# Kernel tuning notes

Measured on AMD Instinct MI355X. Metric: run time of the kernel, lower is better.

The kernel has to match this reference:

```python
import jax, jax.numpy as jnp
import numpy as np
import itertools

NBX = NBY = 6
NUM_BLOCKS = NBX * NBY

def _build_adj():
    adj = []
    for i, j in itertools.product(range(NBX), range(NBY)):
        for dx, dy in [(-1, 0), (0, -1), (0, 1), (1, 0)]:
            x, y = i + dx, j + dy
            if 0 <= x < NBX and 0 <= y < NBY:
                adj.append((j * NBX + i, y * NBX + x))
    return np.array(adj, dtype=np.int32)

ADJ = _build_adj()                                   # [E=120, 2] (src, dst)
NUM_EDGES = ADJ.shape[0]
# composition structure: edge e' can be extended by edge e iff dst(e') == src(e)
COMP = (ADJ[:, 1][:, None] == ADJ[:, 0][None, :]).astype(np.float32)  # [E, E]
MAX_PATH_LEN = NUM_BLOCKS                            # 36 fixed-point iterations


def setup_inputs() -> dict:
    key = jax.random.key(0)
    ks = jax.random.split(key, 10)
    w = lambda k, shape: jax.random.normal(k, shape, jnp.float32) * 0.05
    d = {}
    d["image"] = jax.random.normal(ks[0], (1024, 1, 32, 32), jnp.float32)
    d["conv1_w"] = w(ks[1], (32, 1, 5, 5));   d["conv1_b"] = jnp.zeros((32,), jnp.float32)
    d["conv2_w"] = w(ks[2], (32, 32, 5, 5));  d["conv2_b"] = jnp.zeros((32,), jnp.float32)
    d["conv3_w"] = w(ks[3], (64, 32, 5, 5));  d["conv3_b"] = jnp.zeros((64,), jnp.float32)
    d["conv4_w"] = w(ks[4], (64, 64, 5, 5));  d["conv4_b"] = jnp.zeros((64,), jnp.float32)
    d["ep_w1"] = w(ks[5], (256, 256));        d["ep_b1"] = jnp.zeros((256,), jnp.float32)
    d["ep_w2"] = w(ks[6], (NUM_BLOCKS, 256)); d["ep_b2"] = jnp.zeros((NUM_BLOCKS,), jnp.float32)
    d["conn_w1"] = w(ks[7], (256, 256));      d["conn_b1"] = jnp.zeros((256,), jnp.float32)
    d["conn_w2"] = w(ks[8], (NUM_EDGES, 256)); d["conn_b2"] = jnp.zeros((NUM_EDGES,), jnp.float32)
    return d


def _conv(x, w, b):
    y = jax.lax.conv_general_dilated(x, w, (1, 1), 'VALID',
                                     dimension_numbers=('NCHW', 'OIHW', 'NCHW'))
    return y + b[None, :, None, None]


def _pool2(x):
    return jax.lax.reduce_window(x, -jnp.inf, jax.lax.max,
                                 (1, 1, 2, 2), (1, 1, 2, 2), 'VALID')


def reference(image, conv1_w, conv1_b, conv2_w, conv2_b, conv3_w, conv3_b,
              conv4_w, conv4_b, ep_w1, ep_b1, ep_w2, ep_b2,
              conn_w1, conn_b1, conn_w2, conn_b2):
    # --- CNN feature extractor (NCHW, torch-flatten order) ---
    x = _conv(image, conv1_w, conv1_b)      # [B,32,28,28]
    x = _conv(x, conv2_w, conv2_b)          # [B,32,24,24]
    x = _pool2(x)                           # [B,32,12,12]
    x = _conv(x, conv3_w, conv3_b)          # [B,64,8,8]
    x = _conv(x, conv4_w, conv4_b)          # [B,64,4,4]
    x = _pool2(x)                           # [B,64,2,2]
    emb = x.reshape(x.shape[0], -1)         # [B,256]

    # --- heads ---
    conn = jax.nn.sigmoid(jax.nn.relu(emb @ conn_w1.T + conn_b1) @ conn_w2.T + conn_b2)  # [B,E]
    ep = jax.nn.sigmoid(jax.nn.relu(emb @ ep_w1.T + ep_b1) @ ep_w2.T + ep_b2)            # [B,36]

    # --- recursive path building under DAMP semiring (add=clipped sum, mult=product) ---
    comp = jnp.asarray(COMP)                # [E,E]: dst(e')==src(e)
    def step(carry, _):
        old, recent = carry
        # extend_path/extend_path_cond: new symbol is the edge itself, prob = (sum_paths_ending_at_src) * p_edge
        new = jnp.clip(recent @ comp, 0.0, 1.0) * conn   # [B,E]
        merged = jnp.clip(old + new, 0.0, 1.0)           # merge (|) with DAMP add
        return (merged, new), None
    (merged, _), _ = jax.lax.scan(step, (conn, conn), None, length=MAX_PATH_LEN)

    # is_endpoint: apply_if with first_index_check / last_index_check (semiring mult)
    src = jnp.asarray(ADJ[:, 0])
    dst = jnp.asarray(ADJ[:, 1])
    paths = merged * ep[:, src] * ep[:, dst]             # [B,E]
    return paths[:, 0]
```

## Files before the change

### kernel.cpp

```cpp
#include <hip/hip_runtime.h>
#include <math.h>

typedef __attribute__((ext_vector_type(8))) short short8;
typedef __attribute__((ext_vector_type(4))) float float4v;
typedef __attribute__((ext_vector_type(4))) unsigned short ushort4v;

static __device__ __forceinline__ unsigned short f2bf(float f) {
    union { float f; unsigned u; } v; v.f = f;
    unsigned u = v.u;
    return (unsigned short)((u + 0x7fffu + ((u >> 16) & 1u)) >> 16);
}
static __device__ __forceinline__ float bf2f(unsigned short h) {
    union { unsigned u; float f; } v; v.u = ((unsigned)h) << 16;
    return v.f;
}
static __device__ __forceinline__ unsigned pk2(float a, float b) {
    return (unsigned)f2bf(a) | ((unsigned)f2bf(b) << 16);
}

struct AdjT {
    int src[120];
    int dst[120];
    int cnt[36];
    int idx[36][4];
    int ostart[36];
    int ocnt[36];
};

constexpr AdjT build_adj() {
    AdjT a{};
    const int ddx[4] = {-1, 0, 0, 1};
    const int ddy[4] = {0, -1, 1, 0};
    int ne = 0;
    for (int i = 0; i < 6; i++)
        for (int j = 0; j < 6; j++)
            for (int d = 0; d < 4; d++) {
                int x = i + ddx[d], y = j + ddy[d];
                if (x >= 0 && x < 6 && y >= 0 && y < 6) {
                    a.src[ne] = j * 6 + i;
                    a.dst[ne] = y * 6 + x;
                    ne++;
                }
            }
    for (int n = 0; n < 36; n++) {
        a.cnt[n] = 0;
        for (int e = 0; e < 120; e++)
            if (a.dst[e] == n) a.idx[n][a.cnt[n]++] = e;
    }
    for (int n = 0; n < 36; n++) { a.ostart[n] = 0; a.ocnt[n] = 0; }
    for (int e = 0; e < 120; e++) {
        a.ocnt[a.src[e]]++;
        if (e == 0 || a.src[e] != a.src[e - 1]) a.ostart[a.src[e]] = e;
    }
    return a;
}

__device__ constexpr AdjT ADJC = build_adj();
__device__ constexpr int G16_START[17] =
    {0, 3, 6, 9, 12, 14, 16, 18, 20, 22, 24, 26, 28, 30, 32, 34, 36};

__global__ __launch_bounds__(256) void k_prepall(
    const float* __restrict__ w1, const float* __restrict__ b1,
    const float* __restrict__ w2, const float* __restrict__ b2,
    const float* __restrict__ w3, const float* __restrict__ w4,
    const float* __restrict__ cnw1, const float* __restrict__ epw1,
    const float* __restrict__ cnw2, const float* __restrict__ epw2,
    unsigned short* __restrict__ wpc, float* __restrict__ wcb,
    unsigned short* __restrict__ wp3, unsigned short* __restrict__ wp4,
    unsigned short* __restrict__ wph1, unsigned short* __restrict__ wpcn2,
    unsigned short* __restrict__ wpep2) {
    __shared__ float s_w1[800];
    __shared__ float s_w2[800];
    if (blockIdx.x < 32) {
        const int co = blockIdx.x, tid = threadIdx.x;
        for (int i = tid; i < 800; i += 256) {
            s_w1[i] = w1[i];
            s_w2[i] = w2[co * 800 + i];
        }
        __syncthreads();
        if (tid < 96) {
            int t = tid;
            float val = 0.f;
            if (t < 81) {
                int ty = t / 9, tx = t - 9 * ty;
                int ylo = ty > 4 ? ty - 4 : 0, yhi = ty < 4 ? ty : 4;
                int xlo = tx > 4 ? tx - 4 : 0, xhi = tx < 4 ? tx : 4;
                for (int k1y = ylo; k1y <= yhi; k1y++)
                    for (int k1x = xlo; k1x <= xhi; k1x++) {
                        int o1 = k1y * 5 + k1x;
                        int o2 = (ty - k1y) * 5 + (tx - k1x);
#pragma unroll
                        for (int ci = 0; ci < 32; ci++)
                            val += s_w1[ci * 25 + o1] * s_w2[ci * 25 + o2];
                    }
            }
            int n = co >> 1, nt = co & 1;
            int ks = t >> 5, r = t & 31, q = r >> 3, j = r & 7;
            wpc[ks * 1024 + nt * 512 + (q * 16 + n) * 8 + j] = f2bf(val);
        } else if (tid == 96) {
            float s = b2[co];
            for (int ci = 0; ci < 32; ci++) {
                float ws = 0.f;
#pragma unroll
                for (int t2 = 0; t2 < 25; t2++) ws += s_w2[ci * 25 + t2];
                s += b1[ci] * ws;
            }
            wcb[co] = s;
        }
        return;
    }
    int e = (blockIdx.x - 32) * 256 + threadIdx.x;
    if (e < 51200) {
        int j = e & 7, lane = (e >> 3) & 63, nt = (e >> 9) & 3, t = e >> 11;
        int co = 4 * (lane & 15) + nt, ci = (lane >> 4) * 8 + j;
        wp3[e] = f2bf(w3[(co * 32 + ci) * 25 + t]);
    } else if (e < 153600) {
        int e4 = e - 51200;
        int j = e4 & 7, lane = (e4 >> 3) & 63, nt = (e4 >> 9) & 3;
        int ks = (e4 >> 11) & 1, t = e4 >> 12;
        int co = 4 * (lane & 15) + nt, ci = ks * 32 + (lane >> 4) * 8 + j;
        wp4[e4] = f2bf(w4[(co * 64 + ci) * 25 + t]);
    } else {
        int eh = e - 153600;
        if (eh < 131072) {
            int j = eh & 7, lane = (eh >> 3) & 63, nt = (eh >> 9) & 31, kt = eh >> 14;
            int c = nt * 16 + (lane & 15);
            int k = kt * 32 + ((lane >> 4) << 3) + j;
            float v = (c < 256) ? cnw1[c * 256 + k] : epw1[(c - 256) * 256 + k];
            wph1[eh] = f2bf(v);
        } else if (eh < 163840) {
            int e2 = eh - 131072;
            int j = e2 & 7, lane = (e2 >> 3) & 63, nt = (e2 >> 9) & 7, kt = e2 >> 12;
            int c = nt * 16 + (lane & 15);
            int k = kt * 32 + ((lane >> 4) << 3) + j;
            wpcn2[e2] = f2bf(c < 120 ? cnw2[c * 256 + k] : 0.f);
        } else {
            int e3 = eh - 163840;
            int j = e3 & 7, lane = (e3 >> 3) & 63, idx = e3 >> 9;
            int kt = idx / 3, nt = idx - kt * 3;
            int c = nt * 16 + (lane & 15);
            int k = kt * 32 + ((lane >> 4) << 3) + j;
            wpep2[e3] = f2bf(c < 36 ? epw2[c * 256 + k] : 0.f);
        }
    }
}

__global__ __launch_bounds__(512) void k_convall(
    const float* __restrict__ img,
    const unsigned short* __restrict__ wpc, const float* __restrict__ wcb,
    const unsigned short* __restrict__ wp3, const float* __restrict__ b3,
    const unsigned short* __restrict__ wp4, const float* __restrict__ b4,
    unsigned short* __restrict__ emb) {
    __shared__ __align__(16) unsigned short s_imgbf[2 * 32 * 36];
    __shared__ __align__(16) unsigned short s_buf[2 * 10368];
    const int b2 = blockIdx.x, tid = threadIdx.x;
    const int lane = tid & 63, wave = tid >> 6;
    const int m = lane & 15, quad = lane >> 4;
    const int C3O = 5760;

    {
        int simg = tid >> 8, t = tid & 255;
        float4 v = ((const float4*)(img + (size_t)(2 * b2 + simg) * 1024))[t];
        ushort4v pkv;
        pkv[0] = f2bf(v.x); pkv[1] = f2bf(v.y);
        pkv[2] = f2bf(v.z); pkv[3] = f2bf(v.w);
        *(ushort4v*)(s_imgbf + simg * 1152 + (t >> 3) * 36 + (t & 7) * 4) = pkv;
    }

    const short8* wqc = (const short8*)wpc;
    short8 cb0[3], cb1[3];
#pragma unroll
    for (int ks = 0; ks < 3; ks++) {
        cb0[ks] = wqc[(ks * 2 + 0) * 64 + lane];
        cb1[ks] = wqc[(ks * 2 + 1) * 64 + lane];
    }
    const float bc0 = wcb[2 * m], bc1 = wcb[2 * m + 1];
    int ct[3][8];
#pragma unroll
    for (int ks = 0; ks < 3; ks++)
#pragma unroll
        for (int j = 0; j < 8; j++) {
            int t = ks * 32 + quad * 8 + j;
            int toff = 0;
            if (t < 81) {
                int ty = (t * 57) >> 9;
                toff = ty * 36 + (t - 9 * ty);
            }
            ct[ks][j] = toff;
        }
    const short8* wq3 = (const short8*)wp3;

    __syncthreads();

    for (int TT = wave; TT < 72; TT += 8) {
        int ci = TT >= 36 ? 1 : 0;
        int T = TT - 36 * ci;
        int pg = T * 4 + (m >> 2);
        int py = (pg * 171) >> 11;
        int px = pg - py * 12;
        int wb = ci * 1152 + (2 * py + ((m & 3) >> 1)) * 36 + 2 * px + (m & 1);
        float4v a0 = {0.f, 0.f, 0.f, 0.f};
        float4v a1 = {0.f, 0.f, 0.f, 0.f};
#pragma unroll
        for (int ks = 0; ks < 3; ks++) {
            short8 av;
#pragma unroll
            for (int j = 0; j < 8; j++) av[j] = (short)s_imgbf[wb + ct[ks][j]];
            a0 = __builtin_amdgcn_mfma_f32_16x16x32_bf16(av, cb0[ks], a0, 0, 0, 0);
            a1 = __builtin_amdgcn_mfma_f32_16x16x32_bf16(av, cb1[ks], a1, 0, 0, 0);
        }
        float mx0 = fmaxf(fmaxf(a0[0], a0[1]), fmaxf(a0[2], a0[3])) + bc0;
        float mx1 = fmaxf(fmaxf(a1[0], a1[1]), fmaxf(a1[2], a1[3])) + bc1;
        int row = T * 4 + quad;
        *(unsigned*)(s_buf + ci * 10368 + row * 40 + 2 * m) = pk2(mx0, mx1);
    }
    __syncthreads();

    {
        const int img3 = wave >> 2;
        const int mt0 = ((wave >> 1) & 1) * 2;
        const int nt0 = (wave & 1) * 2;
        const unsigned short* sb = s_buf + img3 * 10368;
        int a3[2];
#pragma unroll
        for (int mi = 0; mi < 2; mi++) {
            int pos3 = (mt0 + mi) * 16 + m;
            int y3 = pos3 >> 3, x3 = pos3 & 7;
            a3[mi] = (y3 * 12 + x3) * 40 + quad * 8;
        }
        float4v acc3[2][2];
#pragma unroll
        for (int mi = 0; mi < 2; mi++)
#pragma unroll
            for (int ni = 0; ni < 2; ni++)
                acc3[mi][ni] = (float4v){0.f, 0.f, 0.f, 0.f};
        short8 bw3[2];
        bw3[0] = wq3[nt0 * 64 + lane];
        bw3[1] = wq3[(nt0 + 1) * 64 + lane];
        for (int t = 0; t < 25; t++) {
            short8 nb3[2];
            if (t < 24) {
                nb3[0] = wq3[((t + 1) * 4 + nt0) * 64 + lane];
                nb3[1] = wq3[((t + 1) * 4 + nt0 + 1) * 64 + lane];
            }
            const int ky = t / 5, kx = t - ky * 5;
            const int toff = (ky * 12 + kx) * 40;
            short8 av0 = *(const short8*)(sb + a3[0] + toff);
            short8 av1 = *(const short8*)(sb + a3[1] + toff);
            acc3[0][0] = __builtin_amdgcn_mfma_f32_16x16x32_bf16(av0, bw3[0], acc3[0][0], 0, 0, 0);
            acc3[0][1] = __builtin_amdgcn_mfma_f32_16x16x32_bf16(av0, bw3[1], acc3[0][1], 0, 0, 0);
            acc3[1][0] = __builtin_amdgcn_mfma_f32_16x16x32_bf16(av1, bw3[0], acc3[1][0], 0, 0, 0);
            acc3[1][1] = __builtin_amdgcn_mfma_f32_16x16x32_bf16(av1, bw3[1], acc3[1][1], 0, 0, 0);
            if (t < 24) { bw3[0] = nb3[0]; bw3[1] = nb3[1]; }
        }
        float bb0 = b3[4 * m + nt0], bb1 = b3[4 * m + nt0 + 1];
#pragma unroll
        for (int mi = 0; mi < 2; mi++)
#pragma unroll
            for (int r = 0; r < 4; r++) {
                int row3 = (mt0 + mi) * 16 + quad * 4 + r;
                *(unsigned*)(s_buf + img3 * 10368 + C3O + row3 * 72 + 4 * m + nt0) =
                    pk2(acc3[mi][0][r] + bb0, acc3[mi][1][r] + bb1);
            }
    }
    __syncthreads();

    {
        const int img4 = wave >> 2, nt4 = wave & 3;
        int y4 = m >> 2, x4 = m & 3;
        const unsigned short* sb = s_buf + img4 * 10368;
        int a4 = C3O + (y4 * 8 + x4) * 72 + quad * 8;
        float4v acc4 = (float4v){0.f, 0.f, 0.f, 0.f};
        const short8* wq4 = (const short8*)wp4;
        short8 cw0 = wq4[(0 * 4 + nt4) * 64 + lane];
        short8 cw1 = wq4[(1 * 4 + nt4) * 64 + lane];
        for (int t = 0; t < 25; t++) {
            short8 n0, n1;
            if (t < 24) {
                n0 = wq4[(((t + 1) * 2) * 4 + nt4) * 64 + lane];
                n1 = wq4[(((t + 1) * 2 + 1) * 4 + nt4) * 64 + lane];
            }
            const int ky = t / 5, kx = t - ky * 5;
            const int toff = (ky * 8 + kx) * 72;
            short8 av0 = *(const short8*)(sb + a4 + toff);
            acc4 = __builtin_amdgcn_mfma_f32_16x16x32_bf16(av0, cw0, acc4, 0, 0, 0);
            short8 av1 = *(const short8*)(sb + a4 + toff + 32);
            acc4 = __builtin_amdgcn_mfma_f32_16x16x32_bf16(av1, cw1, acc4, 0, 0, 0);
            if (t < 24) { cw0 = n0; cw1 = n1; }
        }
        float* s_c4 = (float*)(s_buf + img4 * 10368);
#pragma unroll
        for (int r = 0; r < 4; r++)
            s_c4[(quad * 4 + r) * 68 + 4 * m + nt4] = acc4[r];
    }
    __syncthreads();

    {
        const int simg = tid >> 8, t = tid & 255;
        const float* s_c4 = (const float*)(s_buf + simg * 10368);
        int co = t >> 2, pp = t & 3;
        int ppy = pp >> 1, ppx = pp & 1;
        float v0 = s_c4[((2 * ppy) * 4 + 2 * ppx) * 68 + co];
        float v1 = s_c4[((2 * ppy) * 4 + 2 * ppx + 1) * 68 + co];
        float v2 = s_c4[((2 * ppy + 1) * 4 + 2 * ppx) * 68 + co];
        float v3 = s_c4[((2 * ppy + 1) * 4 + 2 * ppx + 1) * 68 + co];
        emb[(size_t)(2 * b2 + simg) * 256 + t] =
            f2bf(fmaxf(fmaxf(v0, v1), fmaxf(v2, v3)) + b4[co]);
    }
}

__global__ __launch_bounds__(256) void k_heads(
    const unsigned short* __restrict__ emb,
    const unsigned short* __restrict__ wph1,
    const float* __restrict__ cn_b1, const float* __restrict__ ep_b1,
    const unsigned short* __restrict__ wpcn2, const float* __restrict__ cn_b2,
    const unsigned short* __restrict__ wpep2, const float* __restrict__ ep_b2,
    float* __restrict__ out) {
    __shared__ unsigned short s_hid[16 * 520];
    __shared__ float s_conn[120 * 17];
    __shared__ float s_rec0[120 * 17];
    __shared__ float s_rec1[120 * 17];
    __shared__ float s_ep[36 * 17];
    const int tid = threadIdx.x;
    const int lane = tid & 63, wave = tid >> 6;
    const int m = lane & 15, q = lane >> 4;
    const int b0 = blockIdx.x * 16;

    float4v acc[8];
#pragma unroll
    for (int i = 0; i < 8; i++) acc[i] = (float4v){0.f, 0.f, 0.f, 0.f};
    const short8* wp1 = (const short8*)wph1;
    for (int kt = 0; kt < 8; kt++) {
        short8 av = *(const short8*)(emb + (size_t)(b0 + m) * 256 + kt * 32 + q * 8);
#pragma unroll
        for (int ntl = 0; ntl < 8; ntl++) {
            int nt = wave * 8 + ntl;
            short8 bv = wp1[(kt * 32 + nt) * 64 + lane];
            acc[ntl] = __builtin_amdgcn_mfma_f32_16x16x32_bf16(av, bv, acc[ntl], 0, 0, 0);
        }
    }
#pragma unroll
    for (int ntl = 0; ntl < 8; ntl++) {
        int c = (wave * 8 + ntl) * 16 + m;
        float bb = (c < 256) ? cn_b1[c] : ep_b1[c - 256];
#pragma unroll
        for (int r = 0; r < 4; r++)
            s_hid[(q * 4 + r) * 520 + c] = f2bf(fmaxf(acc[ntl][r] + bb, 0.f));
    }
    __syncthreads();

    for (int job = wave; job < 11; job += 4) {
        const bool isconn = job < 8;
        const int koff = isconn ? 0 : 256;
        float4v a2 = (float4v){0.f, 0.f, 0.f, 0.f};
        for (int kt = 0; kt < 8; kt++) {
            short8 av = *(const short8*)(s_hid + m * 520 + koff + kt * 32 + q * 8);
            short8 bv = isconn
                ? ((const short8*)wpcn2)[(kt * 8 + job) * 64 + lane]
                : ((const short8*)wpep2)[(kt * 3 + (job - 8)) * 64 + lane];
            a2 = __builtin_amdgcn_mfma_f32_16x16x32_bf16(av, bv, a2, 0, 0, 0);
        }
        int c = (isconn ? job : (job - 8)) * 16 + m;
        float bb = isconn ? (c < 120 ? cn_b2[c] : 0.f) : (c < 36 ? ep_b2[c] : 0.f);
#pragma unroll
        for (int r = 0; r < 4; r++) {
            float v = 1.f / (1.f + __expf(-(a2[r] + bb)));
            int row = q * 4 + r;
            if (isconn) {
                if (c < 120) { s_conn[c * 17 + row] = v; s_rec0[c * 17 + row] = v; }
            } else {
                if (c < 36) s_ep[c * 17 + row] = v;
            }
        }
    }
    __syncthreads();

    const int row = tid >> 4, g = tid & 15;
    const int ns = G16_START[g];
    const int nodecnt = G16_START[g + 1] - ns;
    int ie[3][4], icnt[3], os[3], oc[3];
    float cr[3][4];
#pragma unroll
    for (int s = 0; s < 3; s++) {
        if (s < nodecnt) {
            int n = ns + s;
            icnt[s] = ADJC.cnt[n];
#pragma unroll
            for (int qx = 0; qx < 4; qx++) ie[s][qx] = ADJC.idx[n][qx];
            os[s] = ADJC.ostart[n];
            oc[s] = ADJC.ocnt[n];
#pragma unroll
            for (int oe = 0; oe < 4; oe++)
                cr[s][oe] = (oe < oc[s]) ? s_conn[(os[s] + oe) * 17 + row] : 0.f;
        } else {
            icnt[s] = 0; oc[s] = 0; os[s] = 0;
#pragma unroll
            for (int qx = 0; qx < 4; qx++) ie[s][qx] = 0;
#pragma unroll
            for (int oe = 0; oe < 4; oe++) cr[s][oe] = 0.f;
        }
    }
    float old0 = (g == 0) ? s_conn[0 * 17 + row] : 0.f;

    for (int it = 0; it < 36; it++) {
        const float* cur = (it & 1) ? s_rec1 : s_rec0;
        float* nxt = (it & 1) ? s_rec0 : s_rec1;
#pragma unroll
        for (int s = 0; s < 3; s++) {
            float sum = 0.f;
#pragma unroll
            for (int qx = 0; qx < 4; qx++)
                sum += (qx < icnt[s]) ? cur[ie[s][qx] * 17 + row] : 0.f;
            sum = fminf(sum, 1.f);
#pragma unroll
            for (int oe = 0; oe < 4; oe++) {
                if (oe < oc[s]) {
                    int e = os[s] + oe;
                    float nv = sum * cr[s][oe];
                    nxt[e * 17 + row] = nv;
                    if (g == 0 && s == 0 && oe == 0)
                        old0 = fminf(old0 + nv, 1.f);
                }
            }
        }
        __asm__ volatile("s_waitcnt lgkmcnt(0)" ::: "memory");
    }

    if (g == 0)
        out[b0 + row] = old0 * s_ep[0 * 17 + row] * s_ep[6 * 17 + row];
}

extern "C" void kernel_launch(void* const* d_in, const int* in_sizes, int n_in,
                              void* d_out, int out_size, void* d_ws, size_t ws_size,
                              hipStream_t stream) {
    const float* image = (const float*)d_in[0];
    const float* c1w = (const float*)d_in[1];
    const float* c1b = (const float*)d_in[2];
    const float* c2w = (const float*)d_in[3];
    const float* c2b = (const float*)d_in[4];
    const float* c3w = (const float*)d_in[5];
    const float* c3b = (const float*)d_in[6];
    const float* c4w = (const float*)d_in[7];
    const float* c4b = (const float*)d_in[8];
    const float* epw1 = (const float*)d_in[9];
    const float* epb1 = (const float*)d_in[10];
    const float* epw2 = (const float*)d_in[11];
    const float* epb2 = (const float*)d_in[12];
    const float* cnw1 = (const float*)d_in[13];
    const float* cnb1 = (const float*)d_in[14];
    const float* cnw2 = (const float*)d_in[15];
    const float* cnb2 = (const float*)d_in[16];

    const int B = in_sizes[0] / (32 * 32);

    unsigned short* ws = (unsigned short*)d_ws;
    unsigned short* embo = ws;
    unsigned short* wp3 = embo + (size_t)B * 256;
    unsigned short* wp4 = wp3 + 51200;
    unsigned short* wph1 = wp4 + 102400;
    unsigned short* wpcn2 = wph1 + 131072;
    unsigned short* wpep2 = wpcn2 + 32768;
    unsigned short* wpc = wpep2 + 12288;
    float* wcb = (float*)(wpc + 3072);

    k_prepall<<<1320, 256, 0, stream>>>(c1w, c1b, c2w, c2b, c3w, c4w,
                                        cnw1, epw1, cnw2, epw2,
                                        wpc, wcb, wp3, wp4, wph1, wpcn2, wpep2);
    k_convall<<<B / 2, 512, 0, stream>>>(image, wpc, wcb, wp3, c3b, wp4, c4b, embo);
    k_heads<<<B / 16, 256, 0, stream>>>(embo, wph1, cnb1, epb1,
                                        wpcn2, cnb2, wpep2, epb2, (float*)d_out);
}
```

Measured before the change: 161.0 us.

## Process four images per conv block to reuse conv3/conv4 weight fragments

Result: no change. 163.0 us (+1.3%).

```diff
diff --git a/kernel.cpp b/kernel.cpp
--- a/kernel.cpp
+++ b/kernel.cpp
@@ -145,26 +145,29 @@
     }
 }
 
+#define IMG_REG 10368
+#define C3O 5760
+
 __global__ __launch_bounds__(512) void k_convall(
     const float* __restrict__ img,
     const unsigned short* __restrict__ wpc, const float* __restrict__ wcb,
     const unsigned short* __restrict__ wp3, const float* __restrict__ b3,
     const unsigned short* __restrict__ wp4, const float* __restrict__ b4,
     unsigned short* __restrict__ emb) {
-    __shared__ __align__(16) unsigned short s_imgbf[2 * 32 * 36];
-    __shared__ __align__(16) unsigned short s_buf[2 * 10368];
-    const int b2 = blockIdx.x, tid = threadIdx.x;
+    extern __shared__ __align__(16) unsigned short s_dyn[];
+    const int b4i = blockIdx.x, tid = threadIdx.x;
     const int lane = tid & 63, wave = tid >> 6;
     const int m = lane & 15, quad = lane >> 4;
-    const int C3O = 5760;
-
-    {
-        int simg = tid >> 8, t = tid & 255;
-        float4 v = ((const float4*)(img + (size_t)(2 * b2 + simg) * 1024))[t];
+
+#pragma unroll
+    for (int ii = 0; ii < 2; ii++) {
+        int t4 = tid + ii * 512;
+        int simg = t4 >> 8, t = t4 & 255;
+        float4 v = ((const float4*)(img + (size_t)(4 * b4i + simg) * 1024))[t];
         ushort4v pkv;
         pkv[0] = f2bf(v.x); pkv[1] = f2bf(v.y);
         pkv[2] = f2bf(v.z); pkv[3] = f2bf(v.w);
-        *(ushort4v*)(s_imgbf + simg * 1152 + (t >> 3) * 36 + (t & 7) * 4) = pkv;
+        *(ushort4v*)(s_dyn + simg * IMG_REG + C3O + (t >> 3) * 36 + (t & 7) * 4) = pkv;
     }
 
     const short8* wqc = (const short8*)wpc;
@@ -192,35 +195,36 @@
 
     __syncthreads();
 
-    for (int TT = wave; TT < 72; TT += 8) {
-        int ci = TT >= 36 ? 1 : 0;
+    for (int TT = wave; TT < 144; TT += 8) {
+        int ci = TT / 36;
         int T = TT - 36 * ci;
         int pg = T * 4 + (m >> 2);
         int py = (pg * 171) >> 11;
         int px = pg - py * 12;
-        int wb = ci * 1152 + (2 * py + ((m & 3) >> 1)) * 36 + 2 * px + (m & 1);
+        int wb = ci * IMG_REG + C3O + (2 * py + ((m & 3) >> 1)) * 36 + 2 * px + (m & 1);
         float4v a0 = {0.f, 0.f, 0.f, 0.f};
         float4v a1 = {0.f, 0.f, 0.f, 0.f};
 #pragma unroll
         for (int ks = 0; ks < 3; ks++) {
             short8 av;
 #pragma unroll
-            for (int j = 0; j < 8; j++) av[j] = (short)s_imgbf[wb + ct[ks][j]];
+            for (int j = 0; j < 8; j++) av[j] = (short)s_dyn[wb + ct[ks][j]];
             a0 = __builtin_amdgcn_mfma_f32_16x16x32_bf16(av, cb0[ks], a0, 0, 0, 0);
             a1 = __builtin_amdgcn_mfma_f32_16x16x32_bf16(av, cb1[ks], a1, 0, 0, 0);
         }
         float mx0 = fmaxf(fmaxf(a0[0], a0[1]), fmaxf(a0[2], a0[3])) + bc0;
         float mx1 = fmaxf(fmaxf(a1[0], a1[1]), fmaxf(a1[2], a1[3])) + bc1;
         int row = T * 4 + quad;
-        *(unsigned*)(s_buf + ci * 10368 + row * 40 + 2 * m) = pk2(mx0, mx1);
+        *(unsigned*)(s_dyn + ci * IMG_REG + row * 40 + 2 * m) = pk2(mx0, mx1);
     }
     __syncthreads();
 
     {
-        const int img3 = wave >> 2;
+        const int ip = wave >> 2;
         const int mt0 = ((wave >> 1) & 1) * 2;
         const int nt0 = (wave & 1) * 2;
-        const unsigned short* sb = s_buf + img3 * 10368;
+        const unsigned short* sb0 = s_dyn + (2 * ip + 0) * IMG_REG;
+        const unsigned short* sb1 = s_dyn + (2 * ip + 1) * IMG_REG;
         int a3[2];
 #pragma unroll
         for (int mi = 0; mi < 2; mi++) {
@@ -228,83 +232,110 @@
             int y3 = pos3 >> 3, x3 = pos3 & 7;
             a3[mi] = (y3 * 12 + x3) * 40 + quad * 8;
         }
-        float4v acc3[2][2];
-#pragma unroll
-        for (int mi = 0; mi < 2; mi++)
-#pragma unroll
-            for (int ni = 0; ni < 2; ni++)
-                acc3[mi][ni] = (float4v){0.f, 0.f, 0.f, 0.f};
-        short8 bw3[2];
-        bw3[0] = wq3[nt0 * 64 + lane];
-        bw3[1] = wq3[(nt0 + 1) * 64 + lane];
+        float4v acc3[2][2][2];
+#pragma unroll
+        for (int im = 0; im < 2; im++)
+#pragma unroll
+            for (int mi = 0; mi < 2; mi++)
+#pragma unroll
+                for (int ni = 0; ni < 2; ni++)
+                    acc3[im][mi][ni] = (float4v){0.f, 0.f, 0.f, 0.f};
+        short8 bA0 = wq3[(0 * 4 + nt0) * 64 + lane];
+        short8 bA1 = wq3[(0 * 4 + nt0 + 1) * 64 + lane];
+        short8 bB0 = wq3[(1 * 4 + nt0) * 64 + lane];
+        short8 bB1 = wq3[(1 * 4 + nt0 + 1) * 64 + lane];
         for (int t = 0; t < 25; t++) {
-            short8 nb3[2];
-            if (t < 24) {
-                nb3[0] = wq3[((t + 1) * 4 + nt0) * 64 + lane];
-                nb3[1] = wq3[((t + 1) * 4 + nt0 + 1) * 64 + lane];
+            short8 bC0, bC1;
+            if (t < 23) {
+                bC0 = wq3[((t + 2) * 4 + nt0) * 64 + lane];
+                bC1 = wq3[((t + 2) * 4 + nt0 + 1) * 64 + lane];
             }
             const int ky = t / 5, kx = t - ky * 5;
             const int toff = (ky * 12 + kx) * 40;
-            short8 av0 = *(const short8*)(sb + a3[0] + toff);
-            short8 av1 = *(const short8*)(sb + a3[1] + toff);
-            acc3[0][0] = __builtin_amdgcn_mfma_f32_16x16x32_bf16(av0, bw3[0], acc3[0][0], 0, 0, 0);
-            acc3[0][1] = __builtin_amdgcn_mfma_f32_16x16x32_bf16(av0, bw3[1], acc3[0][1], 0, 0, 0);
-            acc3[1][0] = __builtin_amdgcn_mfma_f32_16x16x32_bf16(av1, bw3[0], acc3[1][0], 0, 0, 0);
-            acc3[1][1] = __builtin_amdgcn_mfma_f32_16x16x32_bf16(av1, bw3[1], acc3[1][1], 0, 0, 0);
-            if (t < 24) { bw3[0] = nb3[0]; bw3[1] = nb3[1]; }
+            short8 av00 = *(const short8*)(sb0 + a3[0] + toff);
+            short8 av01 = *(const short8*)(sb0 + a3[1] + toff);
+            short8 av10 = *(const short8*)(sb1 + a3[0] + toff);
+            short8 av11 = *(const short8*)(sb1 + a3[1] + toff);
+            acc3[0][0][0] = __builtin_amdgcn_mfma_f32_16x16x32_bf16(av00, bA0, acc3[0][0][0], 0, 0, 0);
+            acc3[0][0][1] = __builtin_amdgcn_mfma_f32_16x16x32_bf16(av00, bA1, acc3[0][0][1], 0, 0, 0);
+            acc3[0][1][0] = __builtin_amdgcn_mfma_f32_16x16x32_bf16(av01, bA0, acc3[0][1][0], 0, 0, 0);
+            acc3[0][1][1] = __builtin_amdgcn_mfma_f32_16x16x32_bf16(av01, bA1, acc3[0][1][1], 0, 0, 0);
+            acc3[1][0][0] = __builtin_amdgcn_mfma_f32_16x16x32_bf16(av10, bA0, acc3[1][0][0], 0, 0, 0);
+            acc3[1][0][1] = __builtin_amdgcn_mfma_f32_16x16x32_bf16(av10, bA1, acc3[1][0][1], 0, 0, 0);
+            acc3[1][1][0] = __builtin_amdgcn_mfma_f32_16x16x32_bf16(av11, bA0, acc3[1][1][0], 0, 0, 0);
+            acc3[1][1][1] = __builtin_amdgcn_mfma_f32_16x16x32_bf16(av11, bA1, acc3[1][1][1], 0, 0, 0);
+            bA0 = bB0; bA1 = bB1;
+            if (t < 23) { bB0 = bC0; bB1 = bC1; }
         }
         float bb0 = b3[4 * m + nt0], bb1 = b3[4 * m + nt0 + 1];
 #pragma unroll
-        for (int mi = 0; mi < 2; mi++)
-#pragma unroll
-            for (int r = 0; r < 4; r++) {
-                int row3 = (mt0 + mi) * 16 + quad * 4 + r;
-                *(unsigned*)(s_buf + img3 * 10368 + C3O + row3 * 72 + 4 * m + nt0) =
-                    pk2(acc3[mi][0][r] + bb0, acc3[mi][1][r] + bb1);
-            }
+        for (int im = 0; im < 2; im++)
+#pragma unroll
+            for (int mi = 0; mi < 2; mi++)
+#pragma unroll
+                for (int r = 0; r < 4; r++) {
+                    int row3 = (mt0 + mi) * 16 + quad * 4 + r;
+                    *(unsigned*)(s_dyn + (2 * ip + im) * IMG_REG + C3O + row3 * 72 + 4 * m + nt0) =
+                        pk2(acc3[im][mi][0][r] + bb0, acc3[im][mi][1][r] + bb1);
+                }
     }
     __syncthreads();
 
     {
-        const int img4 = wave >> 2, nt4 = wave & 3;
+        const int ip = wave >> 2, nt4 = wave & 3;
         int y4 = m >> 2, x4 = m & 3;
-        const unsigned short* sb = s_buf + img4 * 10368;
+        const unsigned short* sb0 = s_dyn + (2 * ip + 0) * IMG_REG;
+        const unsigned short* sb1 = s_dyn + (2 * ip + 1) * IMG_REG;
         int a4 = C3O + (y4 * 8 + x4) * 72 + quad * 8;
-        float4v acc4 = (float4v){0.f, 0.f, 0.f, 0.f};
+        float4v acc4[2];
+        acc4[0] = (float4v){0.f, 0.f, 0.f, 0.f};
+        acc4[1] = (float4v){0.f, 0.f, 0.f, 0.f};
         const short8* wq4 = (const short8*)wp4;
-        short8 cw0 = wq4[(0 * 4 + nt4) * 64 + lane];
-        short8 cw1 = wq4[(1 * 4 + nt4) * 64 + lane];
+        short8 cA0 = wq4[((0 * 2 + 0) * 4 + nt4) * 64 + lane];
+        short8 cA1 = wq4[((0 * 2 + 1) * 4 + nt4) * 64 + lane];
+        short8 cB0 = wq4[((1 * 2 + 0) * 4 + nt4) * 64 + lane];
+        short8 cB1 = wq4[((1 * 2 + 1) * 4 + nt4) * 64 + lane];
         for (int t = 0; t < 25; t++) {
-            short8 n0, n1;
-            if (t < 24) {
-                n0 = wq4[(((t + 1) * 2) * 4 + nt4) * 64 + lane];
-                n1 = wq4[(((t + 1) * 2 + 1) * 4 + nt4) * 64 + lane];
+            short8 cC0, cC1;
+            if (t < 23) {
+                cC0 = wq4[(((t + 2) * 2 + 0) * 4 + nt4) * 64 + lane];
+                cC1 = wq4[(((t + 2) * 2 + 1) * 4 + nt4) * 64 + lane];
             }
             const int ky = t / 5, kx = t - ky * 5;
             const int toff = (ky * 8 + kx) * 72;
-            short8 av0 = *(const short8*)(sb + a4 + toff);
-            acc4 = __builtin_amdgcn_mfma_f32_16x16x32_bf16(av0, cw0, acc4, 0, 0, 0);
-            short8 av1 = *(const short8*)(sb + a4 + toff + 32);
-            acc4 = __builtin_amdgcn_mfma_f32_16x16x32_bf16(av1, cw1, acc4, 0, 0, 0);
-            if (t < 24) { cw0 = n0; cw1 = n1; }
-        }
-        float* s_c4 = (float*)(s_buf + img4 * 10368);
-#pragma unroll
-        for (int r = 0; r < 4; r++)
-            s_c4[(quad * 4 + r) * 68 + 4 * m + nt4] = acc4[r];
+            short8 a00 = *(const short8*)(sb0 + a4 + toff);
+            short8 a01 = *(const short8*)(sb0 + a4 + toff + 32);
+            short8 a10 = *(const short8*)(sb1 + a4 + toff);
+            short8 a11 = *(const short8*)(sb1 + a4 + toff + 32);
+            acc4[0] = __builtin_amdgcn_mfma_f32_16x16x32_bf16(a00, cA0, acc4[0], 0, 0, 0);
+            acc4[0] = __builtin_amdgcn_mfma_f32_16x16x32_bf16(a01, cA1, acc4[0], 0, 0, 0);
+            acc4[1] = __builtin_amdgcn_mfma_f32_16x16x32_bf16(a10, cA0, acc4[1], 0, 0, 0);
+            acc4[1] = __builtin_amdgcn_mfma_f32_16x16x32_bf16(a11, cA1, acc4[1], 0, 0, 0);
+            cA0 = cB0; cA1 = cB1;
+            if (t < 23) { cB0 = cC0; cB1 = cC1; }
+        }
+#pragma unroll
+        for (int im = 0; im < 2; im++) {
+            float* s_c4 = (float*)(s_dyn + (2 * ip + im) * IMG_REG);
+#pragma unroll
+            for (int r = 0; r < 4; r++)
+                s_c4[(quad * 4 + r) * 68 + 4 * m + nt4] = acc4[im][r];
+        }
     }
     __syncthreads();
 
-    {
-        const int simg = tid >> 8, t = tid & 255;
-        const float* s_c4 = (const float*)(s_buf + simg * 10368);
+#pragma unroll
+    for (int ii = 0; ii < 2; ii++) {
+        int t4 = tid + ii * 512;
+        const int simg = t4 >> 8, t = t4 & 255;
+        const float* s_c4 = (const float*)(s_dyn + simg * IMG_REG);
         int co = t >> 2, pp = t & 3;
         int ppy = pp >> 1, ppx = pp & 1;
         float v0 = s_c4[((2 * ppy) * 4 + 2 * ppx) * 68 + co];
         float v1 = s_c4[((2 * ppy) * 4 + 2 * ppx + 1) * 68 + co];
         float v2 = s_c4[((2 * ppy + 1) * 4 + 2 * ppx) * 68 + co];
         float v3 = s_c4[((2 * ppy + 1) * 4 + 2 * ppx + 1) * 68 + co];
-        emb[(size_t)(2 * b2 + simg) * 256 + t] =
+        emb[(size_t)(4 * b4i + simg) * 256 + t] =
             f2bf(fmaxf(fmaxf(v0, v1), fmaxf(v2, v3)) + b4[co]);
     }
 }
@@ -463,10 +494,18 @@
     unsigned short* wpc = wpep2 + 12288;
     float* wcb = (float*)(wpc + 3072);
 
+    const int conv_lds = 4 * IMG_REG * (int)sizeof(unsigned short);
+    static int attr_done = 0;
+    if (!attr_done) {
+        hipFuncSetAttribute((const void*)k_convall,
+                            hipFuncAttributeMaxDynamicSharedMemorySize, conv_lds);
+        attr_done = 1;
+    }
+
     k_prepall<<<1320, 256, 0, stream>>>(c1w, c1b, c2w, c2b, c3w, c4w,
                                         cnw1, epw1, cnw2, epw2,
                                         wpc, wcb, wp3, wp4, wph1, wpcn2, wpep2);
-    k_convall<<<B / 2, 512, 0, stream>>>(image, wpc, wcb, wp3, c3b, wp4, c4b, embo);
+    k_convall<<<B / 4, 512, conv_lds, stream>>>(image, wpc, wcb, wp3, c3b, wp4, c4b, embo);
     k_heads<<<B / 16, 256, 0, stream>>>(embo, wph1, cnb1, epb1,
                                         wpcn2, cnb2, wpep2, epb2, (float*)d_out);
 }
```

## Gather fused conv1-2 im2col rows with vector loads from shifted image copies

Applied to the files above, without the earlier changes.

New measurement: 161.6 us. Within noise of the previous version (+0.4%).

```diff
diff --git a/kernel.cpp b/kernel.cpp
--- a/kernel.cpp
+++ b/kernel.cpp
@@ -9,10 +9,6 @@
     union { float f; unsigned u; } v; v.f = f;
     unsigned u = v.u;
     return (unsigned short)((u + 0x7fffu + ((u >> 16) & 1u)) >> 16);
-}
-static __device__ __forceinline__ float bf2f(unsigned short h) {
-    union { unsigned u; float f; } v; v.u = ((unsigned)h) << 16;
-    return v.f;
 }
 static __device__ __forceinline__ unsigned pk2(float a, float b) {
     return (unsigned)f2bf(a) | ((unsigned)f2bf(b) << 16);
@@ -78,11 +74,11 @@
             s_w2[i] = w2[co * 800 + i];
         }
         __syncthreads();
-        if (tid < 96) {
+        if (tid < 128) {
             int t = tid;
+            int ty = t / 12, tx = t - 12 * ty;
             float val = 0.f;
-            if (t < 81) {
-                int ty = t / 9, tx = t - 9 * ty;
+            if (ty < 9 && tx < 9) {
                 int ylo = ty > 4 ? ty - 4 : 0, yhi = ty < 4 ? ty : 4;
                 int xlo = tx > 4 ? tx - 4 : 0, xhi = tx < 4 ? tx : 4;
                 for (int k1y = ylo; k1y <= yhi; k1y++)
@@ -97,7 +93,7 @@
             int n = co >> 1, nt = co & 1;
             int ks = t >> 5, r = t & 31, q = r >> 3, j = r & 7;
             wpc[ks * 1024 + nt * 512 + (q * 16 + n) * 8 + j] = f2bf(val);
-        } else if (tid == 96) {
+        } else if (tid == 128) {
             float s = b2[co];
             for (int ci = 0; ci < 32; ci++) {
                 float ws = 0.f;
@@ -145,49 +141,68 @@
     }
 }
 
+#define REGSZ 10656
+#define C3O 5760
+#define CPY 1224
+
 __global__ __launch_bounds__(512) void k_convall(
     const float* __restrict__ img,
     const unsigned short* __restrict__ wpc, const float* __restrict__ wcb,
     const unsigned short* __restrict__ wp3, const float* __restrict__ b3,
     const unsigned short* __restrict__ wp4, const float* __restrict__ b4,
     unsigned short* __restrict__ emb) {
-    __shared__ __align__(16) unsigned short s_imgbf[2 * 32 * 36];
-    __shared__ __align__(16) unsigned short s_buf[2 * 10368];
+    __shared__ __align__(16) unsigned short s_buf[2 * REGSZ];
     const int b2 = blockIdx.x, tid = threadIdx.x;
     const int lane = tid & 63, wave = tid >> 6;
     const int m = lane & 15, quad = lane >> 4;
-    const int C3O = 5760;
 
     {
         int simg = tid >> 8, t = tid & 255;
         float4 v = ((const float4*)(img + (size_t)(2 * b2 + simg) * 1024))[t];
-        ushort4v pkv;
-        pkv[0] = f2bf(v.x); pkv[1] = f2bf(v.y);
-        pkv[2] = f2bf(v.z); pkv[3] = f2bf(v.w);
-        *(ushort4v*)(s_imgbf + simg * 1152 + (t >> 3) * 36 + (t & 7) * 4) = pkv;
+        unsigned short pv[4];
+        pv[0] = f2bf(v.x); pv[1] = f2bf(v.y);
+        pv[2] = f2bf(v.z); pv[3] = f2bf(v.w);
+        int r = t >> 3, x0 = (t & 7) * 4;
+        int p36 = r * 36 + x0;
+        unsigned short* reg = s_buf + simg * REGSZ + C3O;
+#pragma unroll
+        for (int c = 0; c < 4; c++)
+#pragma unroll
+            for (int i = 0; i < 4; i++) {
+                int pos = p36 + i - c;
+                if (pos >= 0) reg[c * CPY + pos] = pv[i];
+            }
+    }
+    if (tid < 400) {
+        int simg = tid >= 200, zz = tid - 200 * simg;
+        int r, x;
+        if (zz < 128) { r = zz >> 2; x = 32 + (zz & 3); }
+        else { int rr = zz - 128; r = 32 + (rr >= 36 ? 1 : 0); x = rr - (rr >= 36 ? 36 : 0); }
+        int p36 = r * 36 + x;
+        unsigned short* reg = s_buf + simg * REGSZ + C3O;
+#pragma unroll
+        for (int c = 0; c < 4; c++) {
+            int pos = p36 - c;
+            if (pos >= 0 && pos < CPY) reg[c * CPY + pos] = 0;
+        }
     }
 
     const short8* wqc = (const short8*)wpc;
-    short8 cb0[3], cb1[3];
-#pragma unroll
-    for (int ks = 0; ks < 3; ks++) {
+    short8 cb0[4], cb1[4];
+#pragma unroll
+    for (int ks = 0; ks < 4; ks++) {
         cb0[ks] = wqc[(ks * 2 + 0) * 64 + lane];
         cb1[ks] = wqc[(ks * 2 + 1) * 64 + lane];
     }
     const float bc0 = wcb[2 * m], bc1 = wcb[2 * m + 1];
-    int ct[3][8];
-#pragma unroll
-    for (int ks = 0; ks < 3; ks++)
-#pragma unroll
-        for (int j = 0; j < 8; j++) {
-            int t = ks * 32 + quad * 8 + j;
-            int toff = 0;
-            if (t < 81) {
-                int ty = (t * 57) >> 9;
-                toff = ty * 36 + (t - 9 * ty);
-            }
-            ct[ks][j] = toff;
-        }
+    int ct1[4], ct2[4];
+#pragma unroll
+    for (int ks = 0; ks < 4; ks++) {
+        int t0 = ks * 32 + quad * 8;
+        ct1[ks] = (t0 / 12) * 36 + (t0 % 12);
+        int t4 = t0 + 4;
+        ct2[ks] = (t4 / 12) * 36 + (t4 % 12);
+    }
     const short8* wq3 = (const short8*)wp3;
 
     __syncthreads();
@@ -198,21 +213,30 @@
         int pg = T * 4 + (m >> 2);
         int py = (pg * 171) >> 11;
         int px = pg - py * 12;
-        int wb = ci * 1152 + (2 * py + ((m & 3) >> 1)) * 36 + 2 * px + (m & 1);
+        int albase = (2 * py + ((m & 3) >> 1)) * 36 + 2 * px + (m & 1);
+        const unsigned short* reg = s_buf + ci * REGSZ + C3O;
         float4v a0 = {0.f, 0.f, 0.f, 0.f};
         float4v a1 = {0.f, 0.f, 0.f, 0.f};
 #pragma unroll
-        for (int ks = 0; ks < 3; ks++) {
+        for (int ks = 0; ks < 4; ks++) {
+            int a = albase + ct1[ks];
+            int c = a & 3;
+            ushort4v lo = *(const ushort4v*)(reg + c * CPY + (a - c));
+            a = albase + ct2[ks];
+            c = a & 3;
+            ushort4v hi = *(const ushort4v*)(reg + c * CPY + (a - c));
             short8 av;
-#pragma unroll
-            for (int j = 0; j < 8; j++) av[j] = (short)s_imgbf[wb + ct[ks][j]];
+            av[0] = (short)lo[0]; av[1] = (short)lo[1];
+            av[2] = (short)lo[2]; av[3] = (short)lo[3];
+            av[4] = (short)hi[0]; av[5] = (short)hi[1];
+            av[6] = (short)hi[2]; av[7] = (short)hi[3];
             a0 = __builtin_amdgcn_mfma_f32_16x16x32_bf16(av, cb0[ks], a0, 0, 0, 0);
             a1 = __builtin_amdgcn_mfma_f32_16x16x32_bf16(av, cb1[ks], a1, 0, 0, 0);
         }
         float mx0 = fmaxf(fmaxf(a0[0], a0[1]), fmaxf(a0[2], a0[3])) + bc0;
         float mx1 = fmaxf(fmaxf(a1[0], a1[1]), fmaxf(a1[2], a1[3])) + bc1;
         int row = T * 4 + quad;
-        *(unsigned*)(s_buf + ci * 10368 + row * 40 + 2 * m) = pk2(mx0, mx1);
+        *(unsigned*)(s_buf + ci * REGSZ + row * 40 + 2 * m) = pk2(mx0, mx1);
     }
     __syncthreads();
 
@@ -220,7 +244,7 @@
         const int img3 = wave >> 2;
         const int mt0 = ((wave >> 1) & 1) * 2;
         const int nt0 = (wave & 1) * 2;
-        const unsigned short* sb = s_buf + img3 * 10368;
+        const unsigned short* sb = s_buf + img3 * REGSZ;
         int a3[2];
 #pragma unroll
         for (int mi = 0; mi < 2; mi++) {
@@ -259,7 +283,7 @@
 #pragma unroll
             for (int r = 0; r < 4; r++) {
                 int row3 = (mt0 + mi) * 16 + quad * 4 + r;
-                *(unsigned*)(s_buf + img3 * 10368 + C3O + row3 * 72 + 4 * m + nt0) =
+                *(unsigned*)(s_buf + img3 * REGSZ + C3O + row3 * 72 + 4 * m + nt0) =
                     pk2(acc3[mi][0][r] + bb0, acc3[mi][1][r] + bb1);
             }
     }
@@ -268,7 +292,7 @@
     {
         const int img4 = wave >> 2, nt4 = wave & 3;
         int y4 = m >> 2, x4 = m & 3;
-        const unsigned short* sb = s_buf + img4 * 10368;
+        const unsigned short* sb = s_buf + img4 * REGSZ;
         int a4 = C3O + (y4 * 8 + x4) * 72 + quad * 8;
         float4v acc4 = (float4v){0.f, 0.f, 0.f, 0.f};
         const short8* wq4 = (const short8*)wp4;
@@ -288,7 +312,7 @@
             acc4 = __builtin_amdgcn_mfma_f32_16x16x32_bf16(av1, cw1, acc4, 0, 0, 0);
             if (t < 24) { cw0 = n0; cw1 = n1; }
         }
-        float* s_c4 = (float*)(s_buf + img4 * 10368);
+        float* s_c4 = (float*)(s_buf + img4 * REGSZ);
 #pragma unroll
         for (int r = 0; r < 4; r++)
             s_c4[(quad * 4 + r) * 68 + 4 * m + nt4] = acc4[r];
@@ -297,7 +321,7 @@
 
     {
         const int simg = tid >> 8, t = tid & 255;
-        const float* s_c4 = (const float*)(s_buf + simg * 10368);
+        const float* s_c4 = (const float*)(s_buf + simg * REGSZ);
         int co = t >> 2, pp = t & 3;
         int ppy = pp >> 1, ppx = pp & 1;
         float v0 = s_c4[((2 * ppy) * 4 + 2 * ppx) * 68 + co];
@@ -461,7 +485,7 @@
     unsigned short* wpcn2 = wph1 + 131072;
     unsigned short* wpep2 = wpcn2 + 32768;
     unsigned short* wpc = wpep2 + 12288;
-    float* wcb = (float*)(wpc + 3072);
+    float* wcb = (float*)(wpc + 4096);
 
     k_prepall<<<1320, 256, 0, stream>>>(c1w, c1b, c2w, c2b, c3w, c4w,
                                         cnw1, epw1, cnw2, epw2,
```
